# Kernel optimization log

Measured on AMD Instinct MI355X. Metric: run time of the kernel, lower is better.

The kernel has to match this reference:

```python
import jax, jax.numpy as jnp
import numpy as np

B, S, OBS, H, A = 256, 128, 256, 1024, 18


def setup_inputs() -> dict:
    key = jax.random.key(0)
    ks = jax.random.split(key, 12)
    sc = lambda fan_in: 1.0 / np.sqrt(fan_in)
    u = lambda k, shape, s: jax.random.uniform(k, shape, jnp.float32, -s, s)
    return {
        "obs": jax.random.normal(ks[0], (B, S, OBS), jnp.float32),
        "hx": jnp.zeros((B, H), jnp.float32),
        "cx": jnp.zeros((B, H), jnp.float32),
        "behaviour_acts": jax.random.randint(ks[1], (B, S, 1), 0, A, jnp.int32),
        "W_body": u(ks[2], (H, OBS), sc(OBS)),
        "b_body": u(ks[3], (H,), sc(OBS)),
        "W_ih": u(ks[4], (4 * H, H), sc(H)),
        "b_ih": u(ks[5], (4 * H,), sc(H)),
        "W_hh": u(ks[6], (4 * H, H), sc(H)),
        "b_hh": u(ks[7], (4 * H,), sc(H)),
        "W_v": u(ks[8], (1, H), sc(H)),
        "b_v": u(ks[9], (1,), sc(H)),
        "W_l": u(ks[10], (A, H), sc(H)),
        "b_l": u(ks[11], (A,), sc(H)),
    }


def reference(obs, hx, cx, behaviour_acts, W_body, b_body, W_ih, b_ih,
              W_hh, b_hh, W_v, b_v, W_l, b_l):
    acts = behaviour_acts.astype(jnp.int32).squeeze(-1)  # [B,S]
    # body MLP: Linear + ReLU
    x = jax.nn.relu(jnp.einsum("bso,ho->bsh", obs, W_body) + b_body)  # [B,S,H]
    # precompute input-to-gate contributions for all timesteps (batched GEMM)
    xg = jnp.einsum("bsh,gh->bsg", x, W_ih) + b_ih  # [B,S,4H]
    xg_t = jnp.swapaxes(xg, 0, 1)  # [S,B,4H]

    def step(carry, g_in):
        h, c = carry
        g = g_in + h @ W_hh.T + b_hh  # [B,4H]
        i, f, gg, o = jnp.split(g, 4, axis=-1)  # torch LSTMCell gate order i,f,g,o
        i = jax.nn.sigmoid(i)
        f = jax.nn.sigmoid(f)
        gg = jnp.tanh(gg)
        o = jax.nn.sigmoid(o)
        c = f * c + i * gg
        h = o * jnp.tanh(c)
        return (h, c), h

    _, hs = jax.lax.scan(step, (hx, cx), xg_t)  # hs: [S,B,H]
    hs = jnp.swapaxes(hs, 0, 1)  # [B,S,H]

    value = jnp.einsum("bsh,vh->bsv", hs, W_v) + b_v  # [B,S,1]
    logits = jnp.einsum("bsh,ah->bsa", hs, W_l) + b_l  # [B,S,A]
    # Categorical(probs=softmax(logits)): dist.logits == log_softmax(logits)
    logp = jax.nn.log_softmax(logits, axis=-1)  # [B,S,A]
    log_prob = jnp.take_along_axis(logp, acts[..., None], axis=-1)  # [B,S,1]
    entropy = -jnp.sum(jnp.exp(logp) * logp, axis=-1, keepdims=True)  # [B,S,1]
    return logp, log_prob, entropy, value
```

## Files before the change

kernel.cpp:

```cpp
#include <hip/hip_runtime.h>

#define AS1 __attribute__((address_space(1)))
#define AS3 __attribute__((address_space(3)))

typedef __attribute__((ext_vector_type(4))) float f32x4;
typedef __attribute__((ext_vector_type(8))) short s16x8;
typedef __attribute__((ext_vector_type(4))) short s16x4;

static constexpr int BB = 256, SS = 128, OBSN = 256, HH = 1024, AN = 18;
static constexpr int MM = BB * SS;
static constexpr int G4 = 4 * HH;

static constexpr int LP_OFF  = MM * AN;
static constexpr int ENT_OFF = LP_OFF + MM;
static constexpr int VAL_OFF = ENT_OFF + MM;

__device__ __forceinline__ short f2bf(float f) {
  unsigned u = __builtin_bit_cast(unsigned, f);
  u += 0x7FFFu + ((u >> 16) & 1u);
  return (short)(u >> 16);
}
__device__ __forceinline__ float bf2f(short s) {
  unsigned u = ((unsigned)(unsigned short)s) << 16;
  return __builtin_bit_cast(float, u);
}
__device__ __forceinline__ void gl_lds16(const void* g, void* l) {
  __builtin_amdgcn_global_load_lds((const AS1 void*)g, (AS3 void*)l, 16, 0, 0);
}
__device__ __forceinline__ float sigf(float x) {
  x = fminf(fmaxf(x, -30.f), 30.f);
  return 1.f / (1.f + __expf(-x));
}
__device__ __forceinline__ float tanhfast(float x) {
  x = fminf(fmaxf(x, -15.f), 15.f);
  float e = __expf(2.f * x);
  return (e - 1.f) / (e + 1.f);
}
__device__ __forceinline__ void cast4(const float* __restrict__ s,
                                      short* __restrict__ d, int i) {
  f32x4 v = ((const f32x4*)s)[i];
  s16x4 o;
  o[0] = f2bf(v[0]); o[1] = f2bf(v[1]); o[2] = f2bf(v[2]); o[3] = f2bf(v[3]);
  ((s16x4*)d)[i] = o;
}

__global__ __launch_bounds__(256) void prep(
    const float* __restrict__ obs, const float* __restrict__ Wb,
    const float* __restrict__ Wih, const float* __restrict__ Whh,
    const float* __restrict__ Wl, const float* __restrict__ Wv,
    const float* __restrict__ bih, const float* __restrict__ bhh,
    const float* __restrict__ hx, const float* __restrict__ cx,
    short* __restrict__ obsb, short* __restrict__ wbo, short* __restrict__ wiho,
    short* __restrict__ whho, short* __restrict__ wlo, short* __restrict__ wvo,
    float* __restrict__ bsum, short* __restrict__ h0o, float* __restrict__ co) {
  int i = blockIdx.x * 256 + threadIdx.x;
  if (i < 2097152) { cast4(obs, obsb, i); return; }
  i -= 2097152;
  if (i < 65536) { cast4(Wb, wbo, i); return; }
  i -= 65536;
  if (i < 1048576) { cast4(Wih, wiho, i); return; }
  i -= 1048576;
  if (i < 1048576) { cast4(Whh, whho, i); return; }
  i -= 1048576;
  if (i < 4608) { cast4(Wl, wlo, i); return; }
  i -= 4608;
  if (i < 256) { cast4(Wv, wvo, i); return; }
  i -= 256;
  if (i < 1024) {
    f32x4 a = ((const f32x4*)bih)[i];
    f32x4 b = ((const f32x4*)bhh)[i];
    ((f32x4*)bsum)[i] = a + b;
    return;
  }
  i -= 1024;
  cast4(hx, h0o, i);
  ((f32x4*)co)[i] = ((const f32x4*)cx)[i];
}

template <int N, int K, bool RELU, int REMAP>
__global__ __launch_bounds__(256, 2) void gemm_bt(
    const short* __restrict__ A, const short* __restrict__ Bw,
    const float* __restrict__ bias, short* __restrict__ C, int t0) {
  __shared__ short lA[128 * 32];
  __shared__ short lB[128 * 32];
  const int tid = threadIdx.x;
  const int lane = tid & 63, wave = tid >> 6;
  const int nTN = N / 128;
  const int tm = blockIdx.x / nTN, tn = blockIdx.x % nTN;

  const int r0 = tid >> 2;
  const int kc = (tid & 3) * 8;

  const int m0 = tm * 128 + r0;
  const int m1 = m0 + 64;
  size_t pr0, pr1;
  if constexpr (REMAP == 1) {
    pr0 = (size_t)((m0 & (BB - 1)) * SS + t0 + (m0 >> 8));
    pr1 = (size_t)((m1 & (BB - 1)) * SS + t0 + (m1 >> 8));
  } else {
    pr0 = (size_t)m0; pr1 = (size_t)m1;
  }
  const short* a0 = A + pr0 * K + kc;
  const short* a1 = A + pr1 * K + kc;
  const short* b0 = Bw + (size_t)(tn * 128 + r0) * K + kc;
  const short* b1 = Bw + (size_t)(tn * 128 + r0 + 64) * K + kc;

  f32x4 acc[4][4];
#pragma unroll
  for (int i = 0; i < 4; ++i)
#pragma unroll
    for (int j = 0; j < 4; ++j) acc[i][j] = {0.f, 0.f, 0.f, 0.f};

  const int wr = (wave >> 1) * 64;
  const int wc = (wave & 1) * 64;
  const int fr = lane & 15;
  const int fk = (lane >> 4) * 8;

  for (int k0 = 0; k0 < K; k0 += 32) {
    __syncthreads();
    gl_lds16(a0 + k0, &lA[tid * 8]);
    gl_lds16(a1 + k0, &lA[2048 + tid * 8]);
    gl_lds16(b0 + k0, &lB[tid * 8]);
    gl_lds16(b1 + k0, &lB[2048 + tid * 8]);
    __syncthreads();
    s16x8 af[4], bfr[4];
#pragma unroll
    for (int i = 0; i < 4; ++i)
      af[i] = *(const s16x8*)&lA[(wr + i * 16 + fr) * 32 + fk];
#pragma unroll
    for (int j = 0; j < 4; ++j)
      bfr[j] = *(const s16x8*)&lB[(wc + j * 16 + fr) * 32 + fk];
#pragma unroll
    for (int i = 0; i < 4; ++i)
#pragma unroll
      for (int j = 0; j < 4; ++j)
        acc[i][j] = __builtin_amdgcn_mfma_f32_16x16x32_bf16(af[i], bfr[j], acc[i][j], 0, 0, 0);
  }

  const int orow = (lane >> 4) * 4;
#pragma unroll
  for (int i = 0; i < 4; ++i) {
#pragma unroll
    for (int j = 0; j < 4; ++j) {
      const int colg = tn * 128 + wc + j * 16 + fr;
      const float bv = bias[colg];
#pragma unroll
      for (int r = 0; r < 4; ++r) {
        const int rowg = tm * 128 + wr + i * 16 + orow + r;
        float v = acc[i][j][r] + bv;
        if (RELU) v = v > 0.f ? v : 0.f;
        C[(size_t)rowg * N + colg] = f2bf(v);
      }
    }
  }
}


#define HLD(o0, o1, a_, b_)                                                   \
  asm volatile("global_load_dwordx4 %0, %2, off offset:" #o0 "\n\t"           \
               "global_load_dwordx4 %1, %2, off offset:" #o1                  \
               : "=v"(a_), "=v"(b_) : "v"(hb) : "memory")

#define CHUNK(kc_, wn_, a_, b_)                                               \
  asm volatile("s_waitcnt vmcnt(" #wn_ ")" ::: "memory");                     \
  __builtin_amdgcn_sched_barrier(0);                                          \
  {                                                                           \
    _Pragma("unroll") for (int j = 0; j < 4; ++j) {                           \
      const int rowb = (j * 16 + fr) << 11;                                   \
      const s16x8 w0 = *(const s16x8*)(smem + rowb +                          \
                                       ((((kc_) * 8 + fh) ^ fr) << 4));       \
      const s16x8 w1 = *(const s16x8*)(smem + rowb +                          \
                                       ((((kc_) * 8 + 4 + fh) ^ fr) << 4));   \
      acc[j] = __builtin_amdgcn_mfma_f32_16x16x32_bf16(a_, w0, acc[j], 0, 0, 0); \
      acc[j] = __builtin_amdgcn_mfma_f32_16x16x32_bf16(b_, w1, acc[j], 0, 0, 0); \
    }                                                                         \
  }

__global__ __launch_bounds__(256, 1) void lstm_scan(
    const short* __restrict__ Whh, const short* __restrict__ xg,
    short* __restrict__ hs, const short* __restrict__ h0,
    float* __restrict__ cst, int* __restrict__ bar, int nsteps, int t0) {
  extern __shared__ char smem[];

  const int tid = threadIdx.x, lane = tid & 63, w = tid >> 6;
  const int bt = blockIdx.x >> 6, ht = blockIdx.x & 63;
  const int b0 = bt * 64, hc0 = ht * 16;
  const int fr = lane & 15, fh = lane >> 4;
  const int brow = b0 + w * 16 + fh * 4;
  const int hcol = hc0 + fr;

  float xgv[4][4];
#pragma unroll
  for (int j = 0; j < 4; ++j)
#pragma unroll
    for (int r = 0; r < 4; ++r)
      xgv[j][r] = bf2f(xg[(size_t)(brow + r) * G4 + j * HH + hcol]);

#pragma unroll 4
  for (int j = 0; j < 32; ++j) {
    const int cid = j * 256 + tid;
    const int r = cid >> 7, cc = cid & 127;
    const int wrow = (r >> 4) * HH + hc0 + (r & 15);
    gl_lds16(Whh + (size_t)wrow * HH + ((size_t)(cc ^ (r & 15)) << 3),
             smem + cid * 16);
  }
  float cv[4];
#pragma unroll
  for (int r = 0; r < 4; ++r) cv[r] = cst[(size_t)(brow + r) * HH + hcol];
  int* flags = bar + bt * 64;
  asm volatile("s_waitcnt vmcnt(0)" ::: "memory");
  __syncthreads();

  for (int sl = 0; sl < nsteps; ++sl) {
    const short* hsrc = (sl == 0) ? h0 : hs + (size_t)(sl - 1) * (BB * HH);
    const short* hb = hsrc + (size_t)(b0 + w * 16 + fr) * HH + fh * 8;

    f32x4 acc[4];
#pragma unroll
    for (int j = 0; j < 4; ++j) acc[j] = {0.f, 0.f, 0.f, 0.f};

    s16x8 hA0, hB0, hA1, hB1, hA2, hB2, hA3, hB3, hA4, hB4, hA5, hB5, hA6, hB6,
        hA7, hB7, hA8, hB8, hA9, hB9, hA10, hB10, hA11, hB11, hA12, hB12,
        hA13, hB13, hA14, hB14, hA15, hB15;
    HLD(0, 64, hA0, hB0);       HLD(128, 192, hA1, hB1);
    HLD(256, 320, hA2, hB2);    HLD(384, 448, hA3, hB3);
    HLD(512, 576, hA4, hB4);    HLD(640, 704, hA5, hB5);
    HLD(768, 832, hA6, hB6);    HLD(896, 960, hA7, hB7);
    HLD(1024, 1088, hA8, hB8);  HLD(1152, 1216, hA9, hB9);
    HLD(1280, 1344, hA10, hB10); HLD(1408, 1472, hA11, hB11);
    HLD(1536, 1600, hA12, hB12); HLD(1664, 1728, hA13, hB13);
    HLD(1792, 1856, hA14, hB14); HLD(1920, 1984, hA15, hB15);

    CHUNK(0, 30, hA0, hB0)   CHUNK(1, 28, hA1, hB1)
    CHUNK(2, 26, hA2, hB2)   CHUNK(3, 24, hA3, hB3)
    CHUNK(4, 22, hA4, hB4)   CHUNK(5, 20, hA5, hB5)
    CHUNK(6, 18, hA6, hB6)   CHUNK(7, 16, hA7, hB7)
    CHUNK(8, 14, hA8, hB8)   CHUNK(9, 12, hA9, hB9)
    CHUNK(10, 10, hA10, hB10) CHUNK(11, 8, hA11, hB11)
    CHUNK(12, 6, hA12, hB12) CHUNK(13, 4, hA13, hB13)
    CHUNK(14, 2, hA14, hB14) CHUNK(15, 0, hA15, hB15)

    short* hdst = hs + (size_t)sl * (BB * HH);
#pragma unroll
    for (int r = 0; r < 4; ++r) {
      const float gi = acc[0][r] + xgv[0][r];
      const float gf = acc[1][r] + xgv[1][r];
      const float gc = acc[2][r] + xgv[2][r];
      const float go = acc[3][r] + xgv[3][r];
      const float cn = sigf(gf) * cv[r] + sigf(gi) * tanhfast(gc);
      cv[r] = cn;
      const unsigned hv = (unsigned)(unsigned short)f2bf(sigf(go) * tanhfast(cn));
      short* hp = hdst + (size_t)(brow + r) * HH + hcol;
      asm volatile("global_store_short %0, %1, off sc0 sc1"
                   :: "v"(hp), "v"(hv) : "memory");
    }
    if (sl + 1 < nsteps) {
      const short* xgb = xg + (size_t)(sl + 1) * BB * G4;
      float xgn[4][4];
#pragma unroll
      for (int j = 0; j < 4; ++j)
#pragma unroll
        for (int r = 0; r < 4; ++r)
          xgn[j][r] = bf2f(xgb[(size_t)(brow + r) * G4 + j * HH + hcol]);
      asm volatile("s_waitcnt vmcnt(16)" ::: "memory");
      __syncthreads();
      const int target = t0 + sl + 1;
      if (tid == 0)
        __hip_atomic_store(&flags[ht], target, __ATOMIC_RELAXED,
                           __HIP_MEMORY_SCOPE_AGENT);
      if (tid < 64) {
        while (__hip_atomic_load(&flags[tid], __ATOMIC_RELAXED,
                                 __HIP_MEMORY_SCOPE_AGENT) < target)
          __builtin_amdgcn_s_sleep(1);
      }
      __syncthreads();
#pragma unroll
      for (int j = 0; j < 4; ++j)
#pragma unroll
        for (int r = 0; r < 4; ++r) xgv[j][r] = xgn[j][r];
    }
  }
#pragma unroll
  for (int r = 0; r < 4; ++r) cst[(size_t)(brow + r) * HH + hcol] = cv[r];
}

__global__ __launch_bounds__(256) void heads_k(
    const short* __restrict__ hs, const short* __restrict__ Wl,
    const float* __restrict__ bl, const short* __restrict__ Wv,
    const float* __restrict__ bv, const int* __restrict__ acts,
    float* __restrict__ out, int t0) {
  const int tid = threadIdx.x, lane = tid & 63, wave = tid >> 6;
  const int r = blockIdx.x * 4 + wave;
  const int sl = r >> 8, b = r & 255;
  const int mg = b * SS + t0 + sl;
  const short* hrow = hs + (size_t)r * HH + lane * 16;
  const s16x8 hv0 = *(const s16x8*)hrow;
  const s16x8 hv1 = *(const s16x8*)(hrow + 8);
  float xv[16];
#pragma unroll
  for (int e = 0; e < 8; ++e) { xv[e] = bf2f(hv0[e]); xv[8 + e] = bf2f(hv1[e]); }

  float lg[19];
#pragma unroll
  for (int j = 0; j < 19; ++j) {
    const short* wp = (j < 18 ? Wl + (size_t)j * HH : Wv) + lane * 16;
    const s16x8 w0 = *(const s16x8*)wp;
    const s16x8 w1 = *(const s16x8*)(wp + 8);
    float s = 0.f;
#pragma unroll
    for (int e = 0; e < 8; ++e) s += xv[e] * bf2f(w0[e]) + xv[8 + e] * bf2f(w1[e]);
#pragma unroll
    for (int d = 32; d >= 1; d >>= 1) s += __shfl_xor(s, d, 64);
    lg[j] = s + (j < 18 ? bl[j] : bv[0]);
  }
  float mx = lg[0];
#pragma unroll
  for (int j = 1; j < 18; ++j) mx = fmaxf(mx, lg[j]);
  float se = 0.f;
#pragma unroll
  for (int j = 0; j < 18; ++j) se += __expf(lg[j] - mx);
  const float lse = __logf(se);
  if (lane == 0) {
    const int act = acts[mg];
    float ent = 0.f, sel = 0.f;
#pragma unroll
    for (int j = 0; j < 18; ++j) {
      const float lp = lg[j] - mx - lse;
      out[(size_t)mg * 18 + j] = lp;
      ent -= __expf(lp) * lp;
      if (j == act) sel = lp;
    }
    out[LP_OFF + mg] = sel;
    out[ENT_OFF + mg] = ent;
    out[VAL_OFF + mg] = lg[18];
  }
}

extern "C" void kernel_launch(void* const* d_in, const int* in_sizes, int n_in,
                              void* d_out, int out_size, void* d_ws, size_t ws_size,
                              hipStream_t stream) {
  const float* obs    = (const float*)d_in[0];
  const float* hx     = (const float*)d_in[1];
  const float* cx     = (const float*)d_in[2];
  const int*   acts   = (const int*)d_in[3];
  const float* W_body = (const float*)d_in[4];
  const float* b_body = (const float*)d_in[5];
  const float* W_ih   = (const float*)d_in[6];
  const float* b_ih   = (const float*)d_in[7];
  const float* W_hh   = (const float*)d_in[8];
  const float* b_hh   = (const float*)d_in[9];
  const float* W_v    = (const float*)d_in[10];
  const float* b_v    = (const float*)d_in[11];
  const float* W_l    = (const float*)d_in[12];
  const float* b_l    = (const float*)d_in[13];
  float* out = (float*)d_out;
  (void)in_sizes; (void)n_in; (void)out_size;

  (void)hipFuncSetAttribute((const void*)lstm_scan,
                            hipFuncAttributeMaxDynamicSharedMemorySize, 131072);

  const size_t FIXED = 36235264ull;
  const size_t PER_C = 3145728ull;
  int chunk = 64;
  while (chunk > 1 && FIXED + (size_t)chunk * PER_C > ws_size) chunk >>= 1;

  char* ws = (char*)d_ws;
  size_t off = 0;
  auto give = [&](size_t bytes) -> char* {
    char* p = ws + off;
    off += (bytes + 255) & ~(size_t)255;
    return p;
  };
  short* wb   = (short*)give((size_t)HH * OBSN * 2);
  short* wih  = (short*)give((size_t)G4 * HH * 2);
  short* whh  = (short*)give((size_t)G4 * HH * 2);
  short* wl   = (short*)give((size_t)AN * HH * 2);
  short* wv   = (short*)give((size_t)HH * 2);
  float* bsum = (float*)give((size_t)G4 * 4);
  short* obsb = (short*)give((size_t)MM * OBSN * 2);
  short* h0b  = (short*)give((size_t)BB * HH * 2);
  short* h1b  = (short*)give((size_t)BB * HH * 2);
  float* cbuf = (float*)give((size_t)BB * HH * 4);
  int*   barb = (int*)give(1024);
  short* xc   = (short*)give((size_t)chunk * BB * HH * 2);
  short* xgc  = (short*)give((size_t)chunk * BB * G4 * 2);
  short* hsc  = (short*)give((size_t)chunk * BB * HH * 2);
  (void)h1b;

  hipMemsetAsync(barb, 0, 1024, stream);

  prep<<<16919, 256, 0, stream>>>(obs, W_body, W_ih, W_hh, W_l, W_v, b_ih, b_hh,
                                  hx, cx, obsb, wb, wih, whh, wl, wv, bsum, h0b, cbuf);

  const int Mc = chunk * BB;
  for (int t0 = 0; t0 < SS; t0 += chunk) {
    gemm_bt<HH, OBSN, true, 1>
        <<<(Mc / 128) * (HH / 128), 256, 0, stream>>>(obsb, wb, b_body, xc, t0);
    gemm_bt<G4, HH, false, 0>
        <<<(Mc / 128) * (G4 / 128), 256, 0, stream>>>(xc, wih, bsum, xgc, 0);
    const short* hprev = (t0 == 0) ? h0b : hsc + (size_t)(chunk - 1) * BB * HH;
    lstm_scan<<<256, 256, 131072, stream>>>(whh, xgc, hsc, hprev, cbuf, barb,
                                            chunk, t0);
    heads_k<<<Mc / 4, 256, 0, stream>>>(hsc, wl, b_l, wv, b_v, acts, out, t0);
  }
}
```

Before: 1.578 ms.

## Add split-K 512-thread LSTM scan with per-wave-row flags, alternate per chunk

```diff
diff --git a/kernel.cpp b/kernel.cpp
--- a/kernel.cpp
+++ b/kernel.cpp
@@ -155,7 +155,6 @@
   }
 }
 
-
 #define HLD(o0, o1, a_, b_)                                                   \
   asm volatile("global_load_dwordx4 %0, %2, off offset:" #o0 "\n\t"           \
                "global_load_dwordx4 %1, %2, off offset:" #o1                  \
@@ -176,14 +175,31 @@
     }                                                                         \
   }
 
-__global__ __launch_bounds__(256, 1) void lstm_scan(
+#define CHUNK9(kc_, wn_, a_, b_)                                              \
+  asm volatile("s_waitcnt vmcnt(" #wn_ ")" ::: "memory");                     \
+  __builtin_amdgcn_sched_barrier(0);                                          \
+  {                                                                           \
+    const int cg = kh * 8 + (kc_);                                            \
+    _Pragma("unroll") for (int j = 0; j < 4; ++j) {                           \
+      const int rowb = (j * 16 + fr) << 11;                                   \
+      const s16x8 w0 = *(const s16x8*)(smem + rowb +                          \
+                                       (((cg * 8 + fh) ^ fr) << 4));          \
+      const s16x8 w1 = *(const s16x8*)(smem + rowb +                          \
+                                       (((cg * 8 + 4 + fh) ^ fr) << 4));      \
+      acc[j] = __builtin_amdgcn_mfma_f32_16x16x32_bf16(a_, w0, acc[j], 0, 0, 0); \
+      acc[j] = __builtin_amdgcn_mfma_f32_16x16x32_bf16(b_, w1, acc[j], 0, 0, 0); \
+    }                                                                         \
+  }
+
+__global__ __launch_bounds__(256, 1) void lstm_scan6(
     const short* __restrict__ Whh, const short* __restrict__ xg,
     short* __restrict__ hs, const short* __restrict__ h0,
     float* __restrict__ cst, int* __restrict__ bar, int nsteps, int t0) {
   extern __shared__ char smem[];
 
   const int tid = threadIdx.x, lane = tid & 63, w = tid >> 6;
-  const int bt = blockIdx.x >> 6, ht = blockIdx.x & 63;
+  const int g = blockIdx.x;
+  const int bt = g >> 6, ht = g & 63;
   const int b0 = bt * 64, hc0 = ht * 16;
   const int fr = lane & 15, fh = lane >> 4;
   const int brow = b0 + w * 16 + fh * 4;
@@ -273,6 +289,7 @@
                                  __HIP_MEMORY_SCOPE_AGENT) < target)
           __builtin_amdgcn_s_sleep(1);
       }
+      asm volatile("s_waitcnt vmcnt(0)" ::: "memory");
       __syncthreads();
 #pragma unroll
       for (int j = 0; j < 4; ++j)
@@ -282,6 +299,119 @@
   }
 #pragma unroll
   for (int r = 0; r < 4; ++r) cst[(size_t)(brow + r) * HH + hcol] = cv[r];
+}
+
+__global__ __launch_bounds__(512, 1) void lstm_scan9(
+    const short* __restrict__ Whh, const short* __restrict__ xg,
+    short* __restrict__ hs, const short* __restrict__ h0,
+    float* __restrict__ cst, int* __restrict__ bar, int nsteps, int t0) {
+  extern __shared__ char smem[];
+  float* accx = (float*)(smem + 131072);
+
+  const int tid = threadIdx.x, lane = tid & 63, w = tid >> 6;
+  const int g = blockIdx.x;
+  const int bt = g >> 6, ht = g & 63;
+  const int b0 = bt * 64, hc0 = ht * 16;
+  const int fr = lane & 15, fh = lane >> 4;
+  const int wr_ = w & 3, kh = w >> 2;
+  const int brow = b0 + wr_ * 16 + fh * 4;
+  const int hcol = hc0 + fr;
+
+  float xgA[4][4], xgB[4][4];
+#pragma unroll
+  for (int j = 0; j < 4; ++j)
+#pragma unroll
+    for (int r = 0; r < 4; ++r)
+      xgA[j][r] = bf2f(xg[(size_t)(brow + r) * G4 + j * HH + hcol]);
+
+#pragma unroll 4
+  for (int j = 0; j < 16; ++j) {
+    const int cid = j * 512 + tid;
+    const int r = cid >> 7, cc = cid & 127;
+    const int wrow = (r >> 4) * HH + hc0 + (r & 15);
+    gl_lds16(Whh + (size_t)wrow * HH + ((size_t)(cc ^ (r & 15)) << 3),
+             smem + cid * 16);
+  }
+  float cv[4];
+#pragma unroll
+  for (int r = 0; r < 4; ++r) cv[r] = cst[(size_t)(brow + r) * HH + hcol];
+  int* flags = bar + bt * 256;
+  const int pollIdx = lane * 4 + wr_;
+  const int myFlag  = ht * 4 + wr_;
+  asm volatile("s_waitcnt vmcnt(0)" ::: "memory");
+  __syncthreads();
+
+#define STEP9(sl_, XGC, XGN)                                                  \
+  {                                                                           \
+    const int sl = (sl_);                                                     \
+    const short* hsrc = sl ? hs + (size_t)(sl - 1) * (BB * HH) : h0;          \
+    const short* hb = hsrc + (size_t)(b0 + wr_ * 16 + fr) * HH + kh * 512 +   \
+                      fh * 8;                                                 \
+    if (sl > 0) {                                                             \
+      const int tgt = t0 + sl;                                                \
+      for (;;) {                                                              \
+        const int v = __hip_atomic_load(&flags[pollIdx], __ATOMIC_RELAXED,    \
+                                        __HIP_MEMORY_SCOPE_AGENT);            \
+        if (__ballot(v >= tgt) == ~0ull) break;                               \
+        __builtin_amdgcn_s_sleep(1);                                          \
+      }                                                                       \
+    }                                                                         \
+    f32x4 acc[4];                                                             \
+    _Pragma("unroll") for (int j = 0; j < 4; ++j) acc[j] = {0.f,0.f,0.f,0.f}; \
+    s16x8 hA0,hB0,hA1,hB1,hA2,hB2,hA3,hB3,hA4,hB4,hA5,hB5,hA6,hB6,hA7,hB7;    \
+    HLD(0, 64, hA0, hB0);     HLD(128, 192, hA1, hB1);                        \
+    HLD(256, 320, hA2, hB2);  HLD(384, 448, hA3, hB3);                        \
+    HLD(512, 576, hA4, hB4);  HLD(640, 704, hA5, hB5);                        \
+    HLD(768, 832, hA6, hB6);  HLD(896, 960, hA7, hB7);                        \
+    {    \
+      const int pn = (sl + 1 < nsteps) ? sl + 1 : sl;                         \
+      const short* xgb = xg + (size_t)pn * BB * G4;                           \
+      _Pragma("unroll") for (int j = 0; j < 4; ++j)                           \
+        _Pragma("unroll") for (int r = 0; r < 4; ++r)                         \
+          XGN[j][r] = bf2f(xgb[(size_t)(brow + r) * G4 + j * HH + hcol]);     \
+    }                                                                         \
+    CHUNK9(0, 30, hA0, hB0)  CHUNK9(1, 28, hA1, hB1)                          \
+    CHUNK9(2, 26, hA2, hB2)  CHUNK9(3, 24, hA3, hB3)                          \
+    CHUNK9(4, 22, hA4, hB4)  CHUNK9(5, 20, hA5, hB5)                          \
+    CHUNK9(6, 18, hA6, hB6)  CHUNK9(7, 16, hA7, hB7)                          \
+    if (w >= 4) {                                                             \
+      _Pragma("unroll") for (int j = 0; j < 4; ++j)                           \
+        _Pragma("unroll") for (int r = 0; r < 4; ++r)                         \
+          accx[j * 1024 + (wr_ * 16 + fh * 4 + r) * 16 + fr] = acc[j][r];     \
+    }                                                                         \
+    __syncthreads();     \
+    if (w < 4) {                                                              \
+      short* hdst = hs + (size_t)sl * (BB * HH);                              \
+      _Pragma("unroll") for (int r = 0; r < 4; ++r) {                         \
+        const int rl = (wr_ * 16 + fh * 4 + r) * 16 + fr;                     \
+        const float gi = acc[0][r] + accx[0 * 1024 + rl] + XGC[0][r];         \
+        const float gf = acc[1][r] + accx[1 * 1024 + rl] + XGC[1][r];         \
+        const float gc = acc[2][r] + accx[2 * 1024 + rl] + XGC[2][r];         \
+        const float go = acc[3][r] + accx[3 * 1024 + rl] + XGC[3][r];         \
+        const float cn = sigf(gf) * cv[r] + sigf(gi) * tanhfast(gc);          \
+        cv[r] = cn;                                                           \
+        const unsigned hv =                                                   \
+            (unsigned)(unsigned short)f2bf(sigf(go) * tanhfast(cn));          \
+        short* hp = hdst + (size_t)(brow + r) * HH + hcol;                    \
+        asm volatile("global_store_short %0, %1, off sc0 sc1"                 \
+                     :: "v"(hp), "v"(hv) : "memory");                         \
+      }                                                                       \
+      asm volatile("s_waitcnt vmcnt(0)" ::: "memory");       \
+      if (lane == 0 && sl + 1 < nsteps)                                       \
+        __hip_atomic_store(&flags[myFlag], t0 + sl + 1, __ATOMIC_RELAXED,     \
+                           __HIP_MEMORY_SCOPE_AGENT);                         \
+    }                                                                         \
+  }
+
+  for (int sl2 = 0; sl2 < nsteps; sl2 += 2) {
+    STEP9(sl2, xgA, xgB)
+    STEP9(sl2 + 1, xgB, xgA)
+  }
+  if (w < 4) {
+#pragma unroll
+    for (int r = 0; r < 4; ++r) cst[(size_t)(brow + r) * HH + hcol] = cv[r];
+  }
+#undef STEP9
 }
 
 __global__ __launch_bounds__(256) void heads_k(
@@ -356,10 +486,12 @@
   float* out = (float*)d_out;
   (void)in_sizes; (void)n_in; (void)out_size;
 
-  (void)hipFuncSetAttribute((const void*)lstm_scan,
+  (void)hipFuncSetAttribute((const void*)lstm_scan6,
                             hipFuncAttributeMaxDynamicSharedMemorySize, 131072);
-
-  const size_t FIXED = 36235264ull;
+  (void)hipFuncSetAttribute((const void*)lstm_scan9,
+                            hipFuncAttributeMaxDynamicSharedMemorySize, 147456);
+
+  const size_t FIXED = 36239360ull;
   const size_t PER_C = 3145728ull;
   int chunk = 64;
   while (chunk > 1 && FIXED + (size_t)chunk * PER_C > ws_size) chunk >>= 1;
@@ -381,26 +513,31 @@
   short* h0b  = (short*)give((size_t)BB * HH * 2);
   short* h1b  = (short*)give((size_t)BB * HH * 2);
   float* cbuf = (float*)give((size_t)BB * HH * 4);
-  int*   barb = (int*)give(1024);
+  int*   barb = (int*)give(4096);
   short* xc   = (short*)give((size_t)chunk * BB * HH * 2);
   short* xgc  = (short*)give((size_t)chunk * BB * G4 * 2);
   short* hsc  = (short*)give((size_t)chunk * BB * HH * 2);
   (void)h1b;
 
-  hipMemsetAsync(barb, 0, 1024, stream);
+  hipMemsetAsync(barb, 0, 4096, stream);
 
   prep<<<16919, 256, 0, stream>>>(obs, W_body, W_ih, W_hh, W_l, W_v, b_ih, b_hh,
                                   hx, cx, obsb, wb, wih, whh, wl, wv, bsum, h0b, cbuf);
 
   const int Mc = chunk * BB;
-  for (int t0 = 0; t0 < SS; t0 += chunk) {
+  int li = 0;
+  for (int t0 = 0; t0 < SS; t0 += chunk, ++li) {
     gemm_bt<HH, OBSN, true, 1>
         <<<(Mc / 128) * (HH / 128), 256, 0, stream>>>(obsb, wb, b_body, xc, t0);
     gemm_bt<G4, HH, false, 0>
         <<<(Mc / 128) * (G4 / 128), 256, 0, stream>>>(xc, wih, bsum, xgc, 0);
     const short* hprev = (t0 == 0) ? h0b : hsc + (size_t)(chunk - 1) * BB * HH;
-    lstm_scan<<<256, 256, 131072, stream>>>(whh, xgc, hsc, hprev, cbuf, barb,
-                                            chunk, t0);
+    if ((li & 1) == 0)
+      lstm_scan6<<<256, 256, 131072, stream>>>(whh, xgc, hsc, hprev, cbuf,
+                                               barb, chunk, t0);
+    else
+      lstm_scan9<<<256, 512, 147456, stream>>>(whh, xgc, hsc, hprev, cbuf,
+                                               barb, chunk, t0);
     heads_k<<<Mc / 4, 256, 0, stream>>>(hsc, wl, b_l, wv, b_v, acts, out, t0);
   }
 }
```

Measured after the change: 1.639 ms. +3.9%, slower.
